# Performance work log

Measured on AMD Instinct MI355X. Metric: run time of the kernel, lower is better.

Reference implementation:

```python
import jax, jax.numpy as jnp
import numpy as np

N = 100000   # nodes
E = 1600000  # edges
NF, EF = 128, 16      # node_features, edge_features
NFIL, EFIL = 64, 32   # node_filters, edge_filters
C = 16                # classes


def setup_inputs() -> dict:
    key = jax.random.key(0)
    ks = jax.random.split(key, 12)
    s = 0.1
    return {
        "x": jax.random.normal(ks[0], (N, NF), jnp.float32),
        "edge_index": jax.random.randint(ks[1], (2, E), 0, N),
        "edge_x": jax.random.normal(ks[2], (E, EF), jnp.float32),
        # edge MLP params
        "W1": jax.random.normal(ks[3], (EF, EFIL), jnp.float32) * s,
        "b1": jnp.zeros((EFIL,), jnp.float32),
        "W2": jax.random.normal(ks[4], (EFIL, 1), jnp.float32) * s,
        "b2": jnp.zeros((1,), jnp.float32),
        # GCN layer params
        "Wc1": jax.random.normal(ks[5], (NF, NFIL), jnp.float32) * s,
        "bc1": jnp.zeros((NFIL,), jnp.float32),
        "Wc2": jax.random.normal(ks[6], (NFIL, C), jnp.float32) * s,
        "bc2": jnp.zeros((C,), jnp.float32),
    }


def gcn_conv(x, src, tgt, w, W, b, n):
    # PyG GCNConv with edge_weight: x @ W, symmetric norm, scatter-add, + bias.
    x = x @ W                                             # [n, out]
    deg = jax.ops.segment_sum(w, tgt, num_segments=n)     # weighted degree incl. self-loops
    dinv = jnp.where(deg > 0, jax.lax.rsqrt(deg), 0.0)
    norm = dinv[src] * w * dinv[tgt]                      # [E+n]
    out = jax.ops.segment_sum(norm[:, None] * x[src], tgt, num_segments=n)
    return out + b


def reference(x, edge_index, edge_x, W1, b1, W2, b2, Wc1, bc1, Wc2, bc2):
    # edge MLP -> scalar attention weight per edge
    h = jax.nn.relu(edge_x @ W1 + b1)
    ew = jax.nn.sigmoid(h @ W2 + b2).reshape(-1)          # [E]
    src, tgt = edge_index[0], edge_index[1]
    # add self-loops with weight 1 (as GCNConv does internally)
    loop = jnp.arange(N)
    src_f = jnp.concatenate([src, loop])
    tgt_f = jnp.concatenate([tgt, loop])
    ew_f = jnp.concatenate([ew, jnp.ones((N,), ew.dtype)])
    h1 = jax.nn.relu(gcn_conv(x, src_f, tgt_f, ew_f, Wc1, bc1, N))
    # dropout omitted: eval mode (F.dropout is identity when training=False)
    h2 = gcn_conv(h1, src_f, tgt_f, ew_f, Wc2, bc2, N)
    return jax.nn.log_softmax(h2, axis=1)
```

## Files before the change

### kernel.cpp

```cpp
#include <hip/hip_runtime.h>
#include <math.h>

#define NFD 128
#define EF_ 16
#define EFIL 32
#define NFIL 64
#define CLS 16

typedef unsigned int uint;

__device__ inline void fma4(float4& a, float s, const float4& w) {
  a.x = fmaf(s, w.x, a.x); a.y = fmaf(s, w.y, a.y);
  a.z = fmaf(s, w.z, a.z); a.w = fmaf(s, w.w, a.w);
}

__device__ inline uint bf16_rn(float f) {
  uint u = __float_as_uint(f);
  return (u + 0x7FFFu + ((u >> 16) & 1u)) >> 16;
}

__global__ void init_kernel(int* __restrict__ cur, int n) {
  int i = blockIdx.x * blockDim.x + threadIdx.x;
  if (i < n) cur[(size_t)i * 8] = 0;
}

__global__ __launch_bounds__(256) void edge_mlp_fill_kernel(
    const float* __restrict__ edge_x, const int* __restrict__ ei,
    const float* __restrict__ W1, const float* __restrict__ b1,
    const float* __restrict__ W2, const float* __restrict__ b2,
    int* __restrict__ cur, uint* __restrict__ slot, int cap, int E) {
  __shared__ __align__(16) float sW1[EF_ * EFIL];
  __shared__ float sb1[EFIL];
  __shared__ float sW2[EFIL];
  __shared__ float sb2v;
  int t = threadIdx.x;
  for (int idx = t; idx < EF_ * EFIL / 4; idx += 256)
    reinterpret_cast<float4*>(sW1)[idx] = reinterpret_cast<const float4*>(W1)[idx];
  if (t < EFIL) { sb1[t] = b1[t]; sW2[t] = W2[t]; }
  if (t == 64) sb2v = b2[0];
  __syncthreads();
  int e = blockIdx.x * 256 + t;
  if (e >= E) return;
  const float4* ex4 = reinterpret_cast<const float4*>(edge_x) + (size_t)e * (EF_ / 4);
  float ex[EF_];
  #pragma unroll
  for (int q = 0; q < EF_ / 4; q++) {
    float4 v = ex4[q];
    ex[4*q+0] = v.x; ex[4*q+1] = v.y; ex[4*q+2] = v.z; ex[4*q+3] = v.w;
  }
  float acc[EFIL];
  #pragma unroll
  for (int j = 0; j < EFIL; j++) acc[j] = sb1[j];
  #pragma unroll
  for (int k = 0; k < EF_; k++) {
    float xk = ex[k];
    #pragma unroll
    for (int j4 = 0; j4 < EFIL / 4; j4++) {
      float4 w = reinterpret_cast<const float4*>(sW1)[k * (EFIL/4) + j4];
      acc[4*j4+0] = fmaf(xk, w.x, acc[4*j4+0]);
      acc[4*j4+1] = fmaf(xk, w.y, acc[4*j4+1]);
      acc[4*j4+2] = fmaf(xk, w.z, acc[4*j4+2]);
      acc[4*j4+3] = fmaf(xk, w.w, acc[4*j4+3]);
    }
  }
  float s = sb2v;
  #pragma unroll
  for (int j = 0; j < EFIL; j++) s = fmaf(fmaxf(acc[j], 0.f), sW2[j], s);
  float sig = 1.0f / (1.0f + __expf(-s));
  int sv = ei[e], tg = ei[(size_t)E + e];
  int pos = atomicAdd(&cur[(size_t)tg * 8], 1);
  if (pos < cap)
    slot[(size_t)tg * cap + pos] = ((bf16_rn(sig) & 0x7FFFu) << 17) | (uint)sv;
}

__global__ __launch_bounds__(256) void dinv_kernel(
    const int* __restrict__ cur, const uint* __restrict__ slot,
    int cap, float* __restrict__ dinv, int n) {
  int t = threadIdx.x;
  int node = blockIdx.x * 16 + (t >> 4);
  if (node >= n) return;
  int j = t & 15;
  int cnt = min(cur[(size_t)node * 8], cap);
  const uint* base = slot + (size_t)node * cap;
  float sum = 0.f;
  for (int p = j; p < cnt; p += 16)
    sum += __uint_as_float((base[p] >> 17) << 16);
  sum += __shfl_xor(sum, 1, 16);
  sum += __shfl_xor(sum, 2, 16);
  sum += __shfl_xor(sum, 4, 16);
  sum += __shfl_xor(sum, 8, 16);
  if (j == 0) dinv[node] = rsqrtf(1.0f + sum);
}

__global__ __launch_bounds__(256) void gemm1_kernel(
    const float* __restrict__ x, const float* __restrict__ Wc1,
    uint* __restrict__ xwb, int n) {
  __shared__ __align__(16) float sW[NFD * NFIL];
  int t = threadIdx.x;
  for (int idx = t; idx < NFD * NFIL / 4; idx += 256)
    reinterpret_cast<float4*>(sW)[idx] = reinterpret_cast<const float4*>(Wc1)[idx];
  __syncthreads();
  int tc = t & 15;
  int tr = t >> 4;
  int nrb = (n + 31) >> 5;
  const float4* sW4 = reinterpret_cast<const float4*>(sW);
  for (int rb = blockIdx.x; rb < nrb; rb += gridDim.x) {
    int r0 = rb * 32 + tr * 2;
    int r1 = r0 + 1;
    int c0 = r0 < n ? r0 : n - 1;
    int c1 = r1 < n ? r1 : n - 1;
    const float4* xr0 = reinterpret_cast<const float4*>(x + (size_t)c0 * NFD);
    const float4* xr1 = reinterpret_cast<const float4*>(x + (size_t)c1 * NFD);
    float4 a0 = {0, 0, 0, 0}, a1 = {0, 0, 0, 0};
    #pragma unroll 4
    for (int k4 = 0; k4 < NFD / 4; k4++) {
      float4 xa = xr0[k4];
      float4 xb = xr1[k4];
      float4 w0 = sW4[(k4*4+0)*16 + tc];
      float4 w1 = sW4[(k4*4+1)*16 + tc];
      float4 w2 = sW4[(k4*4+2)*16 + tc];
      float4 w3 = sW4[(k4*4+3)*16 + tc];
      fma4(a0, xa.x, w0); fma4(a0, xa.y, w1); fma4(a0, xa.z, w2); fma4(a0, xa.w, w3);
      fma4(a1, xb.x, w0); fma4(a1, xb.y, w1); fma4(a1, xb.z, w2); fma4(a1, xb.w, w3);
    }
    if (r0 < n) {
      uint2 o = {bf16_rn(a0.x) | (bf16_rn(a0.y) << 16),
                 bf16_rn(a0.z) | (bf16_rn(a0.w) << 16)};
      reinterpret_cast<uint2*>(xwb + (size_t)r0 * 32)[tc] = o;
    }
    if (r1 < n) {
      uint2 o = {bf16_rn(a1.x) | (bf16_rn(a1.y) << 16),
                 bf16_rn(a1.z) | (bf16_rn(a1.w) << 16)};
      reinterpret_cast<uint2*>(xwb + (size_t)r1 * 32)[tc] = o;
    }
  }
}

__global__ __launch_bounds__(256) void agg1_fused_kernel(
    const int* __restrict__ cur, const uint* __restrict__ slot, int cap,
    const float* __restrict__ dinv, const uint* __restrict__ xwb,
    const float* __restrict__ bc1, const float* __restrict__ Wc2,
    float* __restrict__ yw, int n) {
  __shared__ float sh[16][NFIL + 4];
  __shared__ float sW2[NFIL * CLS];
  __shared__ float sb1[NFIL];
  int t = threadIdx.x;
  for (int i = t; i < NFIL * CLS; i += 256) sW2[i] = Wc2[i];
  if (t < NFIL) sb1[t] = bc1[t];
  __syncthreads();
  int r = t >> 4;
  int node = blockIdx.x * 16 + r;
  int f4 = t & 15;
  bool ok = node < n;
  int nd = ok ? node : 0;
  int cnt = ok ? min(cur[(size_t)nd * 8], cap) : 0;
  const uint* base = slot + (size_t)nd * cap;
  const uint2* xw2 = reinterpret_cast<const uint2*>(xwb);
  float d = ok ? dinv[nd] : 0.f;
  uint2 g = xw2[(size_t)nd * 16 + f4];
  float4 acc = {d * __uint_as_float(g.x << 16),
                d * __uint_as_float(g.x & 0xFFFF0000u),
                d * __uint_as_float(g.y << 16),
                d * __uint_as_float(g.y & 0xFFFF0000u)};
  int p = 0;
  for (; p + 1 < cnt; p += 2) {
    uint v0 = base[p], v1 = base[p + 1];
    int s0 = v0 & 0x1FFFF, s1 = v1 & 0x1FFFF;
    float w0 = __uint_as_float((v0 >> 17) << 16) * dinv[s0];
    float w1 = __uint_as_float((v1 >> 17) << 16) * dinv[s1];
    uint2 g0 = xw2[(size_t)s0 * 16 + f4];
    uint2 g1 = xw2[(size_t)s1 * 16 + f4];
    acc.x = fmaf(w0, __uint_as_float(g0.x << 16), acc.x);
    acc.y = fmaf(w0, __uint_as_float(g0.x & 0xFFFF0000u), acc.y);
    acc.z = fmaf(w0, __uint_as_float(g0.y << 16), acc.z);
    acc.w = fmaf(w0, __uint_as_float(g0.y & 0xFFFF0000u), acc.w);
    acc.x = fmaf(w1, __uint_as_float(g1.x << 16), acc.x);
    acc.y = fmaf(w1, __uint_as_float(g1.x & 0xFFFF0000u), acc.y);
    acc.z = fmaf(w1, __uint_as_float(g1.y << 16), acc.z);
    acc.w = fmaf(w1, __uint_as_float(g1.y & 0xFFFF0000u), acc.w);
  }
  if (p < cnt) {
    uint v0 = base[p];
    int s0 = v0 & 0x1FFFF;
    float w0 = __uint_as_float((v0 >> 17) << 16) * dinv[s0];
    uint2 g0 = xw2[(size_t)s0 * 16 + f4];
    acc.x = fmaf(w0, __uint_as_float(g0.x << 16), acc.x);
    acc.y = fmaf(w0, __uint_as_float(g0.x & 0xFFFF0000u), acc.y);
    acc.z = fmaf(w0, __uint_as_float(g0.y << 16), acc.z);
    acc.w = fmaf(w0, __uint_as_float(g0.y & 0xFFFF0000u), acc.w);
  }
  sh[r][4*f4 + 0] = fmaxf(fmaf(d, acc.x, sb1[4*f4 + 0]), 0.f);
  sh[r][4*f4 + 1] = fmaxf(fmaf(d, acc.y, sb1[4*f4 + 1]), 0.f);
  sh[r][4*f4 + 2] = fmaxf(fmaf(d, acc.z, sb1[4*f4 + 2]), 0.f);
  sh[r][4*f4 + 3] = fmaxf(fmaf(d, acc.w, sb1[4*f4 + 3]), 0.f);
  __syncthreads();
  {
    int j = t & 15;
    float o = 0.f;
    #pragma unroll
    for (int k = 0; k < NFIL; k++) o = fmaf(sh[r][k], sW2[k * CLS + j], o);
    if (ok) yw[(size_t)node * CLS + j] = o;
  }
}

__global__ __launch_bounds__(256) void agg2_fused_kernel(
    const int* __restrict__ cur, const uint* __restrict__ slot, int cap,
    const float* __restrict__ dinv, const float* __restrict__ yw,
    const float* __restrict__ bc2, float* __restrict__ out, int n) {
  __shared__ float sb2[CLS];
  int t = threadIdx.x;
  if (t < CLS) sb2[t] = bc2[t];
  __syncthreads();
  int node = blockIdx.x * 16 + (t >> 4);
  int j = t & 15;
  bool ok = node < n;
  int nd = ok ? node : 0;
  int cnt = ok ? min(cur[(size_t)nd * 8], cap) : 0;
  const uint* base = slot + (size_t)nd * cap;
  float d = ok ? dinv[nd] : 0.f;
  float acc = d * yw[(size_t)nd * CLS + j];
  int p = 0;
  for (; p + 1 < cnt; p += 2) {
    uint v0 = base[p], v1 = base[p + 1];
    int s0 = v0 & 0x1FFFF, s1 = v1 & 0x1FFFF;
    float w0 = __uint_as_float((v0 >> 17) << 16) * dinv[s0];
    float w1 = __uint_as_float((v1 >> 17) << 16) * dinv[s1];
    float y0 = yw[(size_t)s0 * CLS + j];
    float y1 = yw[(size_t)s1 * CLS + j];
    acc = fmaf(w0, y0, acc);
    acc = fmaf(w1, y1, acc);
  }
  if (p < cnt) {
    uint v0 = base[p];
    int s0 = v0 & 0x1FFFF;
    float w0 = __uint_as_float((v0 >> 17) << 16) * dinv[s0];
    acc = fmaf(w0, yw[(size_t)s0 * CLS + j], acc);
  }
  float v = fmaf(d, acc, sb2[j]);
  float m = v;
  m = fmaxf(m, __shfl_xor(m, 1, 16));
  m = fmaxf(m, __shfl_xor(m, 2, 16));
  m = fmaxf(m, __shfl_xor(m, 4, 16));
  m = fmaxf(m, __shfl_xor(m, 8, 16));
  float ex = __expf(v - m);
  float ssum = ex;
  ssum += __shfl_xor(ssum, 1, 16);
  ssum += __shfl_xor(ssum, 2, 16);
  ssum += __shfl_xor(ssum, 4, 16);
  ssum += __shfl_xor(ssum, 8, 16);
  if (ok) out[(size_t)node * CLS + j] = (v - m) - __logf(ssum);
}

extern "C" void kernel_launch(void* const* d_in, const int* in_sizes, int n_in,
                              void* d_out, int out_size, void* d_ws, size_t ws_size,
                              hipStream_t stream) {
  const float* x      = (const float*)d_in[0];
  const int*   ei     = (const int*)d_in[1];
  const float* edge_x = (const float*)d_in[2];
  const float* W1     = (const float*)d_in[3];
  const float* b1     = (const float*)d_in[4];
  const float* W2     = (const float*)d_in[5];
  const float* b2     = (const float*)d_in[6];
  const float* Wc1    = (const float*)d_in[7];
  const float* bc1    = (const float*)d_in[8];
  const float* Wc2    = (const float*)d_in[9];
  const float* bc2    = (const float*)d_in[10];
  float* outp = (float*)d_out;
  int n = in_sizes[0] / NFD;
  int E = in_sizes[1] / 2;

  int cap = 64;
  while (cap > 48 && (size_t)n * (4 * (size_t)cap + 228) > ws_size) cap -= 8;

  char* base = (char*)d_ws;
  uint* slot = (uint*)base;          base += (size_t)n * cap * 4;
  int* cur = (int*)base;             base += (size_t)n * 32;
  float* dinv = (float*)base;        base += (size_t)n * 4;
  uint* xwb = (uint*)base;           base += (size_t)n * 128;
  float* yw = (float*)base;
  float* out2 = outp;

  int nblk = (n + 15) / 16;
  init_kernel<<<(n + 255) / 256, 256, 0, stream>>>(cur, n);
  edge_mlp_fill_kernel<<<(E + 255) / 256, 256, 0, stream>>>(
      edge_x, ei, W1, b1, W2, b2, cur, slot, cap, E);
  dinv_kernel<<<nblk, 256, 0, stream>>>(cur, slot, cap, dinv, n);
  gemm1_kernel<<<1024, 256, 0, stream>>>(x, Wc1, xwb, n);
  agg1_fused_kernel<<<nblk, 256, 0, stream>>>(cur, slot, cap, dinv, xwb, bc1, Wc2, yw, n);
  agg2_fused_kernel<<<nblk, 256, 0, stream>>>(cur, slot, cap, dinv, yw, bc2, out2, n);
}
```

Baseline: 224.4 us.

## Replace per-node slot atomics with two-level binning into compact CSR groups

Edges are first binned by target-node range, 2048 nodes per bin, using block-local shared histograms plus one global atomic per bin. A per-bin group kernel then builds a compact CSR-like layout, computing degrees and dinv in shared memory, which replaces the fixed-capacity per-node slot array and the separate dinv kernel. The intermediate layer-2 features are also stored as bf16 to halve gather traffic. This adds an 8-byte staging buffer and an extra pass over it, and the fixed per-bin capacity (CAPB) could drop edges if bins overflow.

```diff
diff --git a/kernel.cpp b/kernel.cpp
--- a/kernel.cpp
+++ b/kernel.cpp
@@ -7,7 +7,14 @@
 #define NFIL 64
 #define CLS 16
 
+#define BSH2 11
+#define NPB2 2048
+#define CAPB 36864
+#define NBX  64
+
 typedef unsigned int uint;
+typedef unsigned long long ull;
+typedef unsigned short ushort;
 
 __device__ inline void fma4(float4& a, float s, const float4& w) {
   a.x = fmaf(s, w.x, a.x); a.y = fmaf(s, w.y, a.y);
@@ -18,78 +25,139 @@
   uint u = __float_as_uint(f);
   return (u + 0x7FFFu + ((u >> 16) & 1u)) >> 16;
 }
-
-__global__ void init_kernel(int* __restrict__ cur, int n) {
+__device__ inline float bf16_tof(uint h) { return __uint_as_float(h << 16); }
+
+__global__ void init_kernel(int* __restrict__ cur, int total) {
   int i = blockIdx.x * blockDim.x + threadIdx.x;
-  if (i < n) cur[(size_t)i * 8] = 0;
-}
-
-__global__ __launch_bounds__(256) void edge_mlp_fill_kernel(
+  if (i < total) cur[i] = 0;
+}
+
+__global__ __launch_bounds__(256) void edge_mlp_bin_kernel(
     const float* __restrict__ edge_x, const int* __restrict__ ei,
     const float* __restrict__ W1, const float* __restrict__ b1,
     const float* __restrict__ W2, const float* __restrict__ b2,
-    int* __restrict__ cur, uint* __restrict__ slot, int cap, int E) {
+    int* __restrict__ bin_cur, ull* __restrict__ binbuf, int E) {
   __shared__ __align__(16) float sW1[EF_ * EFIL];
   __shared__ float sb1[EFIL];
   __shared__ float sW2[EFIL];
   __shared__ float sb2v;
+  __shared__ int hist[NBX];
+  __shared__ int basearr[NBX];
   int t = threadIdx.x;
   for (int idx = t; idx < EF_ * EFIL / 4; idx += 256)
     reinterpret_cast<float4*>(sW1)[idx] = reinterpret_cast<const float4*>(W1)[idx];
   if (t < EFIL) { sb1[t] = b1[t]; sW2[t] = W2[t]; }
   if (t == 64) sb2v = b2[0];
+  if (t >= 128 && t < 128 + NBX) hist[t - 128] = 0;
   __syncthreads();
   int e = blockIdx.x * 256 + t;
-  if (e >= E) return;
-  const float4* ex4 = reinterpret_cast<const float4*>(edge_x) + (size_t)e * (EF_ / 4);
-  float ex[EF_];
-  #pragma unroll
-  for (int q = 0; q < EF_ / 4; q++) {
-    float4 v = ex4[q];
-    ex[4*q+0] = v.x; ex[4*q+1] = v.y; ex[4*q+2] = v.z; ex[4*q+3] = v.w;
-  }
-  float acc[EFIL];
-  #pragma unroll
-  for (int j = 0; j < EFIL; j++) acc[j] = sb1[j];
-  #pragma unroll
-  for (int k = 0; k < EF_; k++) {
-    float xk = ex[k];
-    #pragma unroll
-    for (int j4 = 0; j4 < EFIL / 4; j4++) {
-      float4 w = reinterpret_cast<const float4*>(sW1)[k * (EFIL/4) + j4];
-      acc[4*j4+0] = fmaf(xk, w.x, acc[4*j4+0]);
-      acc[4*j4+1] = fmaf(xk, w.y, acc[4*j4+1]);
-      acc[4*j4+2] = fmaf(xk, w.z, acc[4*j4+2]);
-      acc[4*j4+3] = fmaf(xk, w.w, acc[4*j4+3]);
-    }
-  }
-  float s = sb2v;
-  #pragma unroll
-  for (int j = 0; j < EFIL; j++) s = fmaf(fmaxf(acc[j], 0.f), sW2[j], s);
-  float sig = 1.0f / (1.0f + __expf(-s));
-  int sv = ei[e], tg = ei[(size_t)E + e];
-  int pos = atomicAdd(&cur[(size_t)tg * 8], 1);
-  if (pos < cap)
-    slot[(size_t)tg * cap + pos] = ((bf16_rn(sig) & 0x7FFFu) << 17) | (uint)sv;
-}
-
-__global__ __launch_bounds__(256) void dinv_kernel(
-    const int* __restrict__ cur, const uint* __restrict__ slot,
-    int cap, float* __restrict__ dinv, int n) {
-  int t = threadIdx.x;
-  int node = blockIdx.x * 16 + (t >> 4);
-  if (node >= n) return;
-  int j = t & 15;
-  int cnt = min(cur[(size_t)node * 8], cap);
-  const uint* base = slot + (size_t)node * cap;
-  float sum = 0.f;
-  for (int p = j; p < cnt; p += 16)
-    sum += __uint_as_float((base[p] >> 17) << 16);
-  sum += __shfl_xor(sum, 1, 16);
-  sum += __shfl_xor(sum, 2, 16);
-  sum += __shfl_xor(sum, 4, 16);
-  sum += __shfl_xor(sum, 8, 16);
-  if (j == 0) dinv[node] = rsqrtf(1.0f + sum);
+  bool valid = e < E;
+  float sig = 0.f;
+  int bin = 0, pl = 0;
+  uint lo = 0;
+  if (valid) {
+    const float4* ex4 = reinterpret_cast<const float4*>(edge_x) + (size_t)e * (EF_ / 4);
+    float ex[EF_];
+    #pragma unroll
+    for (int q = 0; q < EF_ / 4; q++) {
+      float4 v = ex4[q];
+      ex[4*q+0] = v.x; ex[4*q+1] = v.y; ex[4*q+2] = v.z; ex[4*q+3] = v.w;
+    }
+    float acc[EFIL];
+    #pragma unroll
+    for (int j = 0; j < EFIL; j++) acc[j] = sb1[j];
+    #pragma unroll
+    for (int k = 0; k < EF_; k++) {
+      float xk = ex[k];
+      #pragma unroll
+      for (int j4 = 0; j4 < EFIL / 4; j4++) {
+        float4 w = reinterpret_cast<const float4*>(sW1)[k * (EFIL/4) + j4];
+        acc[4*j4+0] = fmaf(xk, w.x, acc[4*j4+0]);
+        acc[4*j4+1] = fmaf(xk, w.y, acc[4*j4+1]);
+        acc[4*j4+2] = fmaf(xk, w.z, acc[4*j4+2]);
+        acc[4*j4+3] = fmaf(xk, w.w, acc[4*j4+3]);
+      }
+    }
+    float s = sb2v;
+    #pragma unroll
+    for (int j = 0; j < EFIL; j++) s = fmaf(fmaxf(acc[j], 0.f), sW2[j], s);
+    sig = 1.0f / (1.0f + __expf(-s));
+    int sv = ei[e], tg = ei[(size_t)E + e];
+    bin = tg >> BSH2;
+    lo = (uint)sv | ((uint)(tg & (NPB2 - 1)) << 17);
+    pl = atomicAdd(&hist[bin], 1);
+  }
+  __syncthreads();
+  if (t < NBX) {
+    int c = hist[t];
+    basearr[t] = c ? atomicAdd(&bin_cur[t * 8], c) : 0;
+  }
+  __syncthreads();
+  if (valid) {
+    int pos = basearr[bin] + pl;
+    if (pos < CAPB)
+      binbuf[(size_t)bin * CAPB + pos] = ((ull)__float_as_uint(sig) << 32) | lo;
+  }
+}
+
+__global__ __launch_bounds__(1024) void group_kernel(
+    const int* __restrict__ bin_cur, const ull* __restrict__ binbuf,
+    uint* __restrict__ grp, int* __restrict__ grp_start,
+    int* __restrict__ grp_cnt, float* __restrict__ dinv, int n) {
+  __shared__ int hcnt[NPB2];
+  __shared__ float hsum[NPB2];
+  __shared__ int hpos[NPB2];
+  __shared__ int sd[1024];
+  int b = blockIdx.x, t = threadIdx.x;
+  for (int i = t; i < NPB2; i += 1024) { hcnt[i] = 0; hsum[i] = 0.f; }
+  __syncthreads();
+  int cnt = min(bin_cur[b * 8], CAPB);
+  const ull* eb = binbuf + (size_t)b * CAPB;
+  for (int p = t; p < cnt; p += 1024) {
+    ull v = eb[p];
+    uint lo = (uint)v;
+    int tl = (lo >> 17) & (NPB2 - 1);
+    uint wb = bf16_rn(__uint_as_float((uint)(v >> 32)));
+    atomicAdd(&hcnt[tl], 1);
+    atomicAdd(&hsum[tl], bf16_tof(wb));
+  }
+  __syncthreads();
+  int a0 = hcnt[2*t], a1 = hcnt[2*t + 1];
+  sd[t] = a0 + a1;
+  __syncthreads();
+  for (int off = 1; off < 1024; off <<= 1) {
+    int x = (t >= off) ? sd[t - off] : 0;
+    __syncthreads();
+    sd[t] += x;
+    __syncthreads();
+  }
+  int ex = sd[t] - (a0 + a1);
+  __syncthreads();
+  int node0 = b * NPB2 + 2*t;
+  if (node0 < n) {
+    grp_start[node0] = b * CAPB + ex;
+    grp_cnt[node0] = a0;
+    dinv[node0] = rsqrtf(1.0f + hsum[2*t]);
+  }
+  if (node0 + 1 < n) {
+    grp_start[node0 + 1] = b * CAPB + ex + a0;
+    grp_cnt[node0 + 1] = a1;
+    dinv[node0 + 1] = rsqrtf(1.0f + hsum[2*t + 1]);
+  }
+  hcnt[2*t] = ex;
+  hcnt[2*t + 1] = ex + a0;
+  hpos[2*t] = 0;
+  hpos[2*t + 1] = 0;
+  __syncthreads();
+  for (int p = t; p < cnt; p += 1024) {
+    ull v = eb[p];
+    uint lo = (uint)v;
+    int tl = (lo >> 17) & (NPB2 - 1);
+    uint src = lo & 0x1FFFFu;
+    uint wb = bf16_rn(__uint_as_float((uint)(v >> 32))) & 0x7FFFu;
+    int pos = hcnt[tl] + atomicAdd(&hpos[tl], 1);
+    grp[(size_t)b * CAPB + pos] = (wb << 17) | src;
+  }
 }
 
 __global__ __launch_bounds__(256) void gemm1_kernel(
@@ -137,10 +205,10 @@
 }
 
 __global__ __launch_bounds__(256) void agg1_fused_kernel(
-    const int* __restrict__ cur, const uint* __restrict__ slot, int cap,
-    const float* __restrict__ dinv, const uint* __restrict__ xwb,
-    const float* __restrict__ bc1, const float* __restrict__ Wc2,
-    float* __restrict__ yw, int n) {
+    const int* __restrict__ grp_start, const int* __restrict__ grp_cnt,
+    const uint* __restrict__ grp, const float* __restrict__ dinv,
+    const uint* __restrict__ xwb, const float* __restrict__ bc1,
+    const float* __restrict__ Wc2, ushort* __restrict__ ywb, int n) {
   __shared__ float sh[16][NFIL + 4];
   __shared__ float sW2[NFIL * CLS];
   __shared__ float sb1[NFIL];
@@ -153,8 +221,8 @@
   int f4 = t & 15;
   bool ok = node < n;
   int nd = ok ? node : 0;
-  int cnt = ok ? min(cur[(size_t)nd * 8], cap) : 0;
-  const uint* base = slot + (size_t)nd * cap;
+  int cnt = ok ? grp_cnt[nd] : 0;
+  const uint* base = grp + (ok ? grp_start[nd] : 0);
   const uint2* xw2 = reinterpret_cast<const uint2*>(xwb);
   float d = ok ? dinv[nd] : 0.f;
   uint2 g = xw2[(size_t)nd * 16 + f4];
@@ -199,14 +267,15 @@
     float o = 0.f;
     #pragma unroll
     for (int k = 0; k < NFIL; k++) o = fmaf(sh[r][k], sW2[k * CLS + j], o);
-    if (ok) yw[(size_t)node * CLS + j] = o;
+    if (ok) ywb[(size_t)node * CLS + j] = (ushort)bf16_rn(o);
   }
 }
 
 __global__ __launch_bounds__(256) void agg2_fused_kernel(
-    const int* __restrict__ cur, const uint* __restrict__ slot, int cap,
-    const float* __restrict__ dinv, const float* __restrict__ yw,
-    const float* __restrict__ bc2, float* __restrict__ out, int n) {
+    const int* __restrict__ grp_start, const int* __restrict__ grp_cnt,
+    const uint* __restrict__ grp, const float* __restrict__ dinv,
+    const ushort* __restrict__ ywb, const float* __restrict__ bc2,
+    float* __restrict__ out, int n) {
   __shared__ float sb2[CLS];
   int t = threadIdx.x;
   if (t < CLS) sb2[t] = bc2[t];
@@ -215,18 +284,18 @@
   int j = t & 15;
   bool ok = node < n;
   int nd = ok ? node : 0;
-  int cnt = ok ? min(cur[(size_t)nd * 8], cap) : 0;
-  const uint* base = slot + (size_t)nd * cap;
+  int cnt = ok ? grp_cnt[nd] : 0;
+  const uint* base = grp + (ok ? grp_start[nd] : 0);
   float d = ok ? dinv[nd] : 0.f;
-  float acc = d * yw[(size_t)nd * CLS + j];
+  float acc = d * bf16_tof(ywb[(size_t)nd * CLS + j]);
   int p = 0;
   for (; p + 1 < cnt; p += 2) {
     uint v0 = base[p], v1 = base[p + 1];
     int s0 = v0 & 0x1FFFF, s1 = v1 & 0x1FFFF;
     float w0 = __uint_as_float((v0 >> 17) << 16) * dinv[s0];
     float w1 = __uint_as_float((v1 >> 17) << 16) * dinv[s1];
-    float y0 = yw[(size_t)s0 * CLS + j];
-    float y1 = yw[(size_t)s1 * CLS + j];
+    float y0 = bf16_tof(ywb[(size_t)s0 * CLS + j]);
+    float y1 = bf16_tof(ywb[(size_t)s1 * CLS + j]);
     acc = fmaf(w0, y0, acc);
     acc = fmaf(w1, y1, acc);
   }
@@ -234,7 +303,7 @@
     uint v0 = base[p];
     int s0 = v0 & 0x1FFFF;
     float w0 = __uint_as_float((v0 >> 17) << 16) * dinv[s0];
-    acc = fmaf(w0, yw[(size_t)s0 * CLS + j], acc);
+    acc = fmaf(w0, bf16_tof(ywb[(size_t)s0 * CLS + j]), acc);
   }
   float v = fmaf(d, acc, sb2[j]);
   float m = v;
@@ -268,24 +337,27 @@
   float* outp = (float*)d_out;
   int n = in_sizes[0] / NFD;
   int E = in_sizes[1] / 2;
-
-  int cap = 64;
-  while (cap > 48 && (size_t)n * (4 * (size_t)cap + 228) > ws_size) cap -= 8;
+  int nbins = (n + NPB2 - 1) >> BSH2;
 
   char* base = (char*)d_ws;
-  uint* slot = (uint*)base;          base += (size_t)n * cap * 4;
-  int* cur = (int*)base;             base += (size_t)n * 32;
-  float* dinv = (float*)base;        base += (size_t)n * 4;
-  uint* xwb = (uint*)base;           base += (size_t)n * 128;
-  float* yw = (float*)base;
-  float* out2 = outp;
+  ull* binbuf = (ull*)base;        base += (size_t)nbins * CAPB * 8;
+  uint* grp = (uint*)base;         base += (size_t)nbins * CAPB * 4;
+  int* bin_cur = (int*)base;       base += (size_t)nbins * 32;
+  int* grp_start = (int*)base;     base += (size_t)n * 4;
+  int* grp_cnt = (int*)base;       base += (size_t)n * 4;
+  float* dinv = (float*)base;      base += (size_t)n * 4;
+  uint* xwb = (uint*)base;         base += (size_t)n * 128;
+  ushort* ywb = (ushort*)base;
 
   int nblk = (n + 15) / 16;
-  init_kernel<<<(n + 255) / 256, 256, 0, stream>>>(cur, n);
-  edge_mlp_fill_kernel<<<(E + 255) / 256, 256, 0, stream>>>(
-      edge_x, ei, W1, b1, W2, b2, cur, slot, cap, E);
-  dinv_kernel<<<nblk, 256, 0, stream>>>(cur, slot, cap, dinv, n);
+  init_kernel<<<(nbins * 8 + 255) / 256, 256, 0, stream>>>(bin_cur, nbins * 8);
+  edge_mlp_bin_kernel<<<(E + 255) / 256, 256, 0, stream>>>(
+      edge_x, ei, W1, b1, W2, b2, bin_cur, binbuf, E);
+  group_kernel<<<nbins, 1024, 0, stream>>>(bin_cur, binbuf, grp, grp_start,
+                                           grp_cnt, dinv, n);
   gemm1_kernel<<<1024, 256, 0, stream>>>(x, Wc1, xwb, n);
-  agg1_fused_kernel<<<nblk, 256, 0, stream>>>(cur, slot, cap, dinv, xwb, bc1, Wc2, yw, n);
-  agg2_fused_kernel<<<nblk, 256, 0, stream>>>(cur, slot, cap, dinv, yw, bc2, out2, n);
-}
+  agg1_fused_kernel<<<nblk, 256, 0, stream>>>(grp_start, grp_cnt, grp, dinv,
+                                              xwb, bc1, Wc2, ywb, n);
+  agg2_fused_kernel<<<nblk, 256, 0, stream>>>(grp_start, grp_cnt, grp, dinv,
+                                              ywb, bc2, outp, n);
+}
```

Measured after the change: 333.5 us. +48.6%, slower.

## Build per-node edge lists via atomic linked lists and store layer-2 features as bf16

Applied to the files above, without the earlier changes.

Replaces the per-target atomicAdd slot fill with an atomicExch linked-list build: each edge records its predecessor in a next buffer, and a walk kernel traverses each node's chain to pack compacted slots, count entries and compute dinv. Layer-1 output projected by Wc2 is now stored as bf16 to halve gather traffic in the second aggregation. The aim is to avoid scattered slot writes during the edge pass and to shrink bandwidth, at the cost of a serial, latency-bound pointer chase per node, extra bf16 rounding, and a cap lowered to 48 that can drop edges for high-degree nodes.

```diff
diff --git a/kernel.cpp b/kernel.cpp
--- a/kernel.cpp
+++ b/kernel.cpp
@@ -8,6 +8,8 @@
 #define CLS 16
 
 typedef unsigned int uint;
+typedef unsigned long long ull;
+typedef unsigned short ushort;
 
 __device__ inline void fma4(float4& a, float s, const float4& w) {
   a.x = fmaf(s, w.x, a.x); a.y = fmaf(s, w.y, a.y);
@@ -18,17 +20,20 @@
   uint u = __float_as_uint(f);
   return (u + 0x7FFFu + ((u >> 16) & 1u)) >> 16;
 }
-
-__global__ void init_kernel(int* __restrict__ cur, int n) {
+__device__ inline float entw(uint lo) {
+  return __uint_as_float((lo >> 17) << 16);
+}
+
+__global__ void init_head_kernel(int* __restrict__ head, int n) {
   int i = blockIdx.x * blockDim.x + threadIdx.x;
-  if (i < n) cur[(size_t)i * 8] = 0;
-}
-
-__global__ __launch_bounds__(256) void edge_mlp_fill_kernel(
+  if (i < n) head[i] = -1;
+}
+
+__global__ __launch_bounds__(256) void edge_mlp_link_kernel(
     const float* __restrict__ edge_x, const int* __restrict__ ei,
     const float* __restrict__ W1, const float* __restrict__ b1,
     const float* __restrict__ W2, const float* __restrict__ b2,
-    int* __restrict__ cur, uint* __restrict__ slot, int cap, int E) {
+    int* __restrict__ head, ull* __restrict__ nextbuf, int E) {
   __shared__ __align__(16) float sW1[EF_ * EFIL];
   __shared__ float sb1[EFIL];
   __shared__ float sW2[EFIL];
@@ -68,28 +73,42 @@
   for (int j = 0; j < EFIL; j++) s = fmaf(fmaxf(acc[j], 0.f), sW2[j], s);
   float sig = 1.0f / (1.0f + __expf(-s));
   int sv = ei[e], tg = ei[(size_t)E + e];
-  int pos = atomicAdd(&cur[(size_t)tg * 8], 1);
-  if (pos < cap)
-    slot[(size_t)tg * cap + pos] = ((bf16_rn(sig) & 0x7FFFu) << 17) | (uint)sv;
-}
-
-__global__ __launch_bounds__(256) void dinv_kernel(
-    const int* __restrict__ cur, const uint* __restrict__ slot,
-    int cap, float* __restrict__ dinv, int n) {
-  int t = threadIdx.x;
-  int node = blockIdx.x * 16 + (t >> 4);
-  if (node >= n) return;
-  int j = t & 15;
-  int cnt = min(cur[(size_t)node * 8], cap);
-  const uint* base = slot + (size_t)node * cap;
+  uint lo = ((bf16_rn(sig) & 0x7FFFu) << 17) | (uint)sv;
+  int old = atomicExch(&head[tg], e);
+  nextbuf[e] = ((ull)(uint)old << 32) | lo;
+}
+
+__global__ __launch_bounds__(256) void walk_kernel(
+    const int* __restrict__ head, const ull* __restrict__ nextbuf,
+    uint* __restrict__ slot, int* __restrict__ grp_cnt,
+    float* __restrict__ dinv, int cap, int n) {
+  int i = blockIdx.x * blockDim.x + threadIdx.x;
+  if (i >= n) return;
+  int e = head[i];
+  int cnt = 0;
   float sum = 0.f;
-  for (int p = j; p < cnt; p += 16)
-    sum += __uint_as_float((base[p] >> 17) << 16);
-  sum += __shfl_xor(sum, 1, 16);
-  sum += __shfl_xor(sum, 2, 16);
-  sum += __shfl_xor(sum, 4, 16);
-  sum += __shfl_xor(sum, 8, 16);
-  if (j == 0) dinv[node] = rsqrtf(1.0f + sum);
+  uint* sl = slot + (size_t)i * cap;
+  while (e >= 0 && cnt < cap) {
+    uint b0 = 0, b1 = 0, b2 = 0, b3 = 0, b4 = 0, b5 = 0, b6 = 0, b7 = 0;
+    int k = 0;
+    ull v;
+    v = nextbuf[e]; b0 = (uint)v; sum += entw(b0); e = (int)(uint)(v >> 32); k = 1;
+    if (e >= 0) { v = nextbuf[e]; b1 = (uint)v; sum += entw(b1); e = (int)(uint)(v >> 32); k = 2;
+    if (e >= 0) { v = nextbuf[e]; b2 = (uint)v; sum += entw(b2); e = (int)(uint)(v >> 32); k = 3;
+    if (e >= 0) { v = nextbuf[e]; b3 = (uint)v; sum += entw(b3); e = (int)(uint)(v >> 32); k = 4;
+    if (e >= 0) { v = nextbuf[e]; b4 = (uint)v; sum += entw(b4); e = (int)(uint)(v >> 32); k = 5;
+    if (e >= 0) { v = nextbuf[e]; b5 = (uint)v; sum += entw(b5); e = (int)(uint)(v >> 32); k = 6;
+    if (e >= 0) { v = nextbuf[e]; b6 = (uint)v; sum += entw(b6); e = (int)(uint)(v >> 32); k = 7;
+    if (e >= 0) { v = nextbuf[e]; b7 = (uint)v; sum += entw(b7); e = (int)(uint)(v >> 32); k = 8;
+    }}}}}}}
+    uint4 lov = {b0, b1, b2, b3};
+    uint4 hiv = {b4, b5, b6, b7};
+    *reinterpret_cast<uint4*>(sl + cnt) = lov;
+    *reinterpret_cast<uint4*>(sl + cnt + 4) = hiv;
+    cnt += k;
+  }
+  grp_cnt[i] = cnt;
+  dinv[i] = rsqrtf(1.0f + sum);
 }
 
 __global__ __launch_bounds__(256) void gemm1_kernel(
@@ -137,10 +156,10 @@
 }
 
 __global__ __launch_bounds__(256) void agg1_fused_kernel(
-    const int* __restrict__ cur, const uint* __restrict__ slot, int cap,
+    const int* __restrict__ grp_cnt, const uint* __restrict__ slot, int cap,
     const float* __restrict__ dinv, const uint* __restrict__ xwb,
     const float* __restrict__ bc1, const float* __restrict__ Wc2,
-    float* __restrict__ yw, int n) {
+    ushort* __restrict__ ywb, int n) {
   __shared__ float sh[16][NFIL + 4];
   __shared__ float sW2[NFIL * CLS];
   __shared__ float sb1[NFIL];
@@ -153,7 +172,7 @@
   int f4 = t & 15;
   bool ok = node < n;
   int nd = ok ? node : 0;
-  int cnt = ok ? min(cur[(size_t)nd * 8], cap) : 0;
+  int cnt = ok ? grp_cnt[nd] : 0;
   const uint* base = slot + (size_t)nd * cap;
   const uint2* xw2 = reinterpret_cast<const uint2*>(xwb);
   float d = ok ? dinv[nd] : 0.f;
@@ -166,8 +185,8 @@
   for (; p + 1 < cnt; p += 2) {
     uint v0 = base[p], v1 = base[p + 1];
     int s0 = v0 & 0x1FFFF, s1 = v1 & 0x1FFFF;
-    float w0 = __uint_as_float((v0 >> 17) << 16) * dinv[s0];
-    float w1 = __uint_as_float((v1 >> 17) << 16) * dinv[s1];
+    float w0 = entw(v0) * dinv[s0];
+    float w1 = entw(v1) * dinv[s1];
     uint2 g0 = xw2[(size_t)s0 * 16 + f4];
     uint2 g1 = xw2[(size_t)s1 * 16 + f4];
     acc.x = fmaf(w0, __uint_as_float(g0.x << 16), acc.x);
@@ -182,7 +201,7 @@
   if (p < cnt) {
     uint v0 = base[p];
     int s0 = v0 & 0x1FFFF;
-    float w0 = __uint_as_float((v0 >> 17) << 16) * dinv[s0];
+    float w0 = entw(v0) * dinv[s0];
     uint2 g0 = xw2[(size_t)s0 * 16 + f4];
     acc.x = fmaf(w0, __uint_as_float(g0.x << 16), acc.x);
     acc.y = fmaf(w0, __uint_as_float(g0.x & 0xFFFF0000u), acc.y);
@@ -199,13 +218,13 @@
     float o = 0.f;
     #pragma unroll
     for (int k = 0; k < NFIL; k++) o = fmaf(sh[r][k], sW2[k * CLS + j], o);
-    if (ok) yw[(size_t)node * CLS + j] = o;
+    if (ok) ywb[(size_t)node * CLS + j] = (ushort)bf16_rn(o);
   }
 }
 
 __global__ __launch_bounds__(256) void agg2_fused_kernel(
-    const int* __restrict__ cur, const uint* __restrict__ slot, int cap,
-    const float* __restrict__ dinv, const float* __restrict__ yw,
+    const int* __restrict__ grp_cnt, const uint* __restrict__ slot, int cap,
+    const float* __restrict__ dinv, const ushort* __restrict__ ywb,
     const float* __restrict__ bc2, float* __restrict__ out, int n) {
   __shared__ float sb2[CLS];
   int t = threadIdx.x;
@@ -215,26 +234,26 @@
   int j = t & 15;
   bool ok = node < n;
   int nd = ok ? node : 0;
-  int cnt = ok ? min(cur[(size_t)nd * 8], cap) : 0;
+  int cnt = ok ? grp_cnt[nd] : 0;
   const uint* base = slot + (size_t)nd * cap;
   float d = ok ? dinv[nd] : 0.f;
-  float acc = d * yw[(size_t)nd * CLS + j];
+  float acc = d * __uint_as_float((uint)ywb[(size_t)nd * CLS + j] << 16);
   int p = 0;
   for (; p + 1 < cnt; p += 2) {
     uint v0 = base[p], v1 = base[p + 1];
     int s0 = v0 & 0x1FFFF, s1 = v1 & 0x1FFFF;
-    float w0 = __uint_as_float((v0 >> 17) << 16) * dinv[s0];
-    float w1 = __uint_as_float((v1 >> 17) << 16) * dinv[s1];
-    float y0 = yw[(size_t)s0 * CLS + j];
-    float y1 = yw[(size_t)s1 * CLS + j];
+    float w0 = entw(v0) * dinv[s0];
+    float w1 = entw(v1) * dinv[s1];
+    float y0 = __uint_as_float((uint)ywb[(size_t)s0 * CLS + j] << 16);
+    float y1 = __uint_as_float((uint)ywb[(size_t)s1 * CLS + j] << 16);
     acc = fmaf(w0, y0, acc);
     acc = fmaf(w1, y1, acc);
   }
   if (p < cnt) {
     uint v0 = base[p];
     int s0 = v0 & 0x1FFFF;
-    float w0 = __uint_as_float((v0 >> 17) << 16) * dinv[s0];
-    acc = fmaf(w0, yw[(size_t)s0 * CLS + j], acc);
+    float w0 = entw(v0) * dinv[s0];
+    acc = fmaf(w0, __uint_as_float((uint)ywb[(size_t)s0 * CLS + j] << 16), acc);
   }
   float v = fmaf(d, acc, sb2[j]);
   float m = v;
@@ -269,23 +288,26 @@
   int n = in_sizes[0] / NFD;
   int E = in_sizes[1] / 2;
 
-  int cap = 64;
-  while (cap > 48 && (size_t)n * (4 * (size_t)cap + 228) > ws_size) cap -= 8;
+  int cap = 48;
+  while (cap > 24 && 8.0 * E + (double)n * (172.0 + 4.0 * cap) > (double)ws_size)
+    cap -= 8;
 
   char* base = (char*)d_ws;
+  int* head = (int*)base;            base += (size_t)n * 4;
+  ull* nextbuf = (ull*)base;         base += (size_t)E * 8;
   uint* slot = (uint*)base;          base += (size_t)n * cap * 4;
-  int* cur = (int*)base;             base += (size_t)n * 32;
+  int* grp_cnt = (int*)base;         base += (size_t)n * 4;
   float* dinv = (float*)base;        base += (size_t)n * 4;
   uint* xwb = (uint*)base;           base += (size_t)n * 128;
-  float* yw = (float*)base;
-  float* out2 = outp;
-
-  int nblk = (n + 15) / 16;
-  init_kernel<<<(n + 255) / 256, 256, 0, stream>>>(cur, n);
-  edge_mlp_fill_kernel<<<(E + 255) / 256, 256, 0, stream>>>(
-      edge_x, ei, W1, b1, W2, b2, cur, slot, cap, E);
-  dinv_kernel<<<nblk, 256, 0, stream>>>(cur, slot, cap, dinv, n);
+  ushort* ywb = (ushort*)base;
+
+  int nblk16 = (n + 15) / 16;
+  int nblk256 = (n + 255) / 256;
+  init_head_kernel<<<nblk256, 256, 0, stream>>>(head, n);
+  edge_mlp_link_kernel<<<(E + 255) / 256, 256, 0, stream>>>(
+      edge_x, ei, W1, b1, W2, b2, head, nextbuf, E);
+  walk_kernel<<<nblk256, 256, 0, stream>>>(head, nextbuf, slot, grp_cnt, dinv, cap, n);
   gemm1_kernel<<<1024, 256, 0, stream>>>(x, Wc1, xwb, n);
-  agg1_fused_kernel<<<nblk, 256, 0, stream>>>(cur, slot, cap, dinv, xwb, bc1, Wc2, yw, n);
-  agg2_fused_kernel<<<nblk, 256, 0, stream>>>(cur, slot, cap, dinv, yw, bc2, out2, n);
-}
+  agg1_fused_kernel<<<nblk16, 256, 0, stream>>>(grp_cnt, slot, cap, dinv, xwb, bc1, Wc2, ywb, n);
+  agg2_fused_kernel<<<nblk16, 256, 0, stream>>>(grp_cnt, slot, cap, dinv, ywb, bc2, outp, n);
+}
```

After: 228.9 us. 1.02x slower.
